# Performance work log

Hardware: AMD Instinct MI355X
Metric: run time of the kernel (lower is better)

## Reference

```python
import jax, jax.numpy as jnp
import numpy as np

LENS = 0.4
DECAY = 0.2
THRESH = 0.2
LOG_SIG_MIN, LOG_SIG_MAX = -20.0, 2.0

# Surrogate-gradient spike: forward is heaviside, backward is rectangular window |x|<lens
@jax.custom_vjp
def act_fun(x):
    return (x > 0.0).astype(x.dtype)

def _act_fwd(x):
    return act_fun(x), x

def _act_bwd(x, g):
    return (g * (jnp.abs(x) < LENS).astype(g.dtype),)

act_fun.defvjp(_act_fwd, _act_bwd)


def _xavier(k, shape):
    fan_out, fan_in = shape
    lim = float(np.sqrt(6.0 / (fan_in + fan_out)))
    return jax.random.uniform(k, shape, jnp.float32, -lim, lim)


def setup_inputs() -> dict:
    key = jax.random.key(0)
    ks = jax.random.split(key, 9)
    B, IN, H, A = 4096, 512, 2048, 32
    return {
        "state": jax.random.normal(ks[0], (B, 5, IN), jnp.float32),
        "W_lif": _xavier(ks[1], (H, IN)), "b_lif": jnp.zeros((H,), jnp.float32),
        "W11": _xavier(ks[2], (H, H)), "b11": jnp.zeros((H,), jnp.float32),
        "W12": _xavier(ks[3], (H, H)), "b12": jnp.zeros((H,), jnp.float32),
        "W21": _xavier(ks[4], (H, H)), "b21": jnp.zeros((H,), jnp.float32),
        "W22": _xavier(ks[5], (H, H)), "b22": jnp.zeros((H,), jnp.float32),
        "Wm": _xavier(ks[6], (A, H)), "bm": jnp.zeros((A,), jnp.float32),
        "Wls": _xavier(ks[7], (A, H)), "bls": jnp.zeros((A,), jnp.float32),
    }


def reference(state, W_lif, b_lif, W11, b11, W12, b12, W21, b21, W22, b22, Wm, bm, Wls, bls):
    x_seq = jnp.repeat(state, 3, axis=1)
    # precompute fc(x) for all steps in one GEMM: [B,15,H]
    fc = jnp.einsum('bti,hi->bth', x_seq, W_lif) + b_lif
    B, T, H = fc.shape

    def step(carry, fc_t):
        mem, spike = carry
        mem1 = mem * DECAY * (1.0 - spike) + fc_t
        spike1 = act_fun(mem1 - THRESH)
        return (mem1, spike1), spike1

    init = (jnp.zeros((B, H), fc.dtype), jnp.zeros((B, H), fc.dtype))
    _, spikes = jax.lax.scan(step, init, jnp.swapaxes(fc, 0, 1))  # [T,B,H]
    x = jnp.mean(spikes, axis=0)  # [B,H]

    x1 = jax.nn.relu(x @ W11.T + b11)
    x1 = jax.nn.relu(x1 @ W12.T + b12)
    mean = x1 @ Wm.T + bm

    x2 = jax.nn.relu(x @ W21.T + b21)
    x2 = jax.nn.relu(x2 @ W22.T + b22)
    log_std = jnp.clip(x2 @ Wls.T + bls, LOG_SIG_MIN, LOG_SIG_MAX)
    return mean, log_std
```

## Files before the change

### kernel.cpp

```cpp
#include <hip/hip_runtime.h>
#include <hip/hip_bf16.h>


typedef _Float16 f16;
using f32x4 = __attribute__((ext_vector_type(4))) float;
using f16x8 = __attribute__((ext_vector_type(8))) f16;

#define MFMA16(a, b, c) __builtin_amdgcn_mfma_f32_16x16x32_f16((a), (b), (c), 0, 0, 0)
#define VMW8()  asm volatile("s_waitcnt vmcnt(8)" ::: "memory")
#define VMW6()  asm volatile("s_waitcnt vmcnt(6)" ::: "memory")
#define VMW0()  asm volatile("s_waitcnt vmcnt(0)" ::: "memory")
#define LGKM0() asm volatile("s_waitcnt lgkmcnt(0)" ::: "memory")
#define BARRIER() __builtin_amdgcn_s_barrier()
#define SCHED0() __builtin_amdgcn_sched_barrier(0)

__device__ __forceinline__ void gload16(const void* g, void* l) {
  __builtin_amdgcn_global_load_lds(
      (const __attribute__((address_space(1))) unsigned int*)g,
      (__attribute__((address_space(3))) unsigned int*)l, 16, 0, 0);
}

__device__ __forceinline__ void cvt8(const float4& a, const float4& b, f16* dst) {
  f16x8 d;
  d[0] = (f16)a.x; d[1] = (f16)a.y; d[2] = (f16)a.z; d[3] = (f16)a.w;
  d[4] = (f16)b.x; d[5] = (f16)b.y; d[6] = (f16)b.z; d[7] = (f16)b.w;
  *(f16x8*)dst = d;
}

__global__ __launch_bounds__(256) void cvt2b_kernel(
    const float* __restrict__ s0, f16* __restrict__ d0, int n8a,
    const float* __restrict__ s1, f16* __restrict__ d1, int n8b)
{
  int i = blockIdx.x * 256 + threadIdx.x;
  const float* src; f16* dst; int k;
  if (i < n8a) { src = s0; dst = d0; k = i; }
  else { k = i - n8a; if (k >= n8b) return; src = s1; dst = d1; }
  const float4* s4 = (const float4*)src;
  float4 a = s4[(size_t)k * 2], b = s4[(size_t)k * 2 + 1];
  cvt8(a, b, dst + (size_t)k * 8);
}

__global__ __launch_bounds__(256) void cvt4_kernel(
    const float* __restrict__ w0, const float* __restrict__ w1,
    const float* __restrict__ w2, const float* __restrict__ w3,
    f16* __restrict__ dst)
{
  int i = blockIdx.x * 256 + threadIdx.x;
  int which = i >> 19, k = i & 524287;
  const float* src = (which == 0) ? w0 : (which == 1) ? w1 : (which == 2) ? w2 : w3;
  const float4* s4 = (const float4*)src;
  float4 a = s4[(size_t)k * 2], b = s4[(size_t)k * 2 + 1];
  cvt8(a, b, dst + (size_t)i * 8);
}

__global__ __launch_bounds__(256) void cvt2_kernel(
    const float* __restrict__ s0, const float* __restrict__ s1,
    f16* __restrict__ d0, f16* __restrict__ d1, int n8each)
{
  int i = blockIdx.x * 256 + threadIdx.x;
  const float* src = (i < n8each) ? s0 : s1;
  f16* dst = (i < n8each) ? d0 : d1;
  int k = (i < n8each) ? i : i - n8each;
  if (k >= n8each) return;
  const float4* s4 = (const float4*)src;
  float4 a = s4[(size_t)k * 2], b = s4[(size_t)k * 2 + 1];
  cvt8(a, b, dst + (size_t)k * 8);
}

__global__ __launch_bounds__(512, 1) void lif256_kernel(
    const f16* __restrict__ S,
    const f16* __restrict__ W,
    const float* __restrict__ bl,
    f16* __restrict__ X)
{
  __shared__ alignas(16) f16 lds[73728];

  const int tid = threadIdx.x, wid = tid >> 6, lane = tid & 63;
  const int wg = ((int)blockIdx.x % 8) * 32 + (int)blockIdx.x / 8;
  const int bn = wg & 15, bm = wg >> 4;
  const int b0 = bm * 256, h0 = bn * 128;
  const int wr0 = (wid >> 1) * 64, wc0 = (wid & 1) * 64;
  const int fr = lane & 15, fq = lane >> 4;
  const int sr = tid >> 3, scb = (tid & 7) * 16;

  f32x4 acc[4][4] = {};
  float mem[4][4][4] = {};
  unsigned pcnt[4][4] = {};

  char* Lb = (char*)&lds[0];
  const int xsw = (fr & 7) << 4;
  const int x0 = (fq * 16) ^ xsw;
  const int x1 = (64 + fq * 16) ^ xsw;
  char* const pA0 = Lb + (wr0 + fr) * 128 + x0;
  char* const pA1 = Lb + (wr0 + fr) * 128 + x1;
  char* const pB0 = Lb + 98304 + (wc0 + fr) * 128 + x0;
  char* const pB1 = Lb + 98304 + (wc0 + fr) * 128 + x1;

  const f16* sBase[4]; const f16* wBase[2];
#pragma unroll
  for (int l = 0; l < 4; ++l) {
    const int row = l * 64 + sr;
    const int c2 = scb ^ ((row & 7) << 4);
    sBase[l] = S + (size_t)(b0 + row) * 2560 + (c2 >> 1);
  }
#pragma unroll
  for (int l = 0; l < 2; ++l) {
    const int row = l * 64 + sr;
    const int c2 = scb ^ ((row & 7) << 4);
    wBase[l] = W + (size_t)(h0 + row) * 512 + (c2 >> 1);
  }

  auto STAGE = [&](int soA, int soB, int g) {
    const int koff = (g >> 3) * 512 + (g & 7) * 64;
    const int kw = (g & 7) * 64;
#pragma unroll
    for (int l = 0; l < 4; ++l)
      gload16(sBase[l] + koff, Lb + soA + l * 8192 + tid * 16);
#pragma unroll
    for (int l = 0; l < 2; ++l)
      gload16(wBase[l] + kw, Lb + 98304 + soB + l * 8192 + tid * 16);
  };

  const float bias[4] = { bl[h0 + wc0 + fr],      bl[h0 + wc0 + 16 + fr],
                          bl[h0 + wc0 + 32 + fr], bl[h0 + wc0 + 48 + fr] };

  STAGE(0, 0, 0);
  STAGE(32768, 16384, 1);
  VMW6();
  BARRIER();
  SCHED0();

  int soA = 0, soB = 0;
  int soStA = 65536, soStB = 32768;
  for (int g = 0; g < 40; ++g) {
    if (g + 2 < 40) STAGE(soStA, soStB, g + 2);
    SCHED0();

    f16x8 b[4][2], a[4][2];
#pragma unroll
    for (int nf = 0; nf < 4; ++nf) {
      b[nf][0] = *(const f16x8*)(pB0 + soB + nf * 2048);
      b[nf][1] = *(const f16x8*)(pB1 + soB + nf * 2048);
    }
#pragma unroll
    for (int mf = 0; mf < 4; ++mf) {
      a[mf][0] = *(const f16x8*)(pA0 + soA + mf * 2048);
      a[mf][1] = *(const f16x8*)(pA1 + soA + mf * 2048);
    }

    __builtin_amdgcn_s_setprio(1);
#pragma unroll
    for (int mf = 0; mf < 4; ++mf)
#pragma unroll
      for (int nf = 0; nf < 4; ++nf) {
        acc[mf][nf] = MFMA16(a[mf][0], b[nf][0], acc[mf][nf]);
        acc[mf][nf] = MFMA16(a[mf][1], b[nf][1], acc[mf][nf]);
      }
    __builtin_amdgcn_s_setprio(0);

    if ((g & 7) == 7) {
#pragma unroll
      for (int mf = 0; mf < 4; ++mf)
#pragma unroll
        for (int nf = 0; nf < 4; ++nf) {
          unsigned pc = pcnt[mf][nf];
#pragma unroll
          for (int r = 0; r < 4; ++r) {
            const float fc = acc[mf][nf][r] + bias[nf];
            float m = mem[mf][nf][r];
            const unsigned inc = 1u << (8 * r);
#pragma unroll
            for (int j = 0; j < 3; ++j) {
              m = ((m > 0.2f) ? 0.f : m * 0.2f) + fc;
              pc += (m > 0.2f) ? inc : 0u;
            }
            mem[mf][nf][r] = m;
          }
          pcnt[mf][nf] = pc;
          acc[mf][nf] = f32x4{0.f, 0.f, 0.f, 0.f};
        }
    }

    LGKM0();
    if (g + 2 < 40)      { VMW6(); }
    else if (g + 1 < 40) { VMW0(); }
    BARRIER();
    SCHED0();

    soA   = (soA   == 65536) ? 0 : soA   + 32768;
    soB   = (soB   == 32768) ? 0 : soB   + 16384;
    soStA = (soStA == 65536) ? 0 : soStA + 32768;
    soStB = (soStB == 32768) ? 0 : soStB + 16384;
  }

#pragma unroll
  for (int nf = 0; nf < 4; ++nf) {
    const int col = h0 + wc0 + nf * 16 + fr;
#pragma unroll
    for (int mf = 0; mf < 4; ++mf) {
      const int row0 = b0 + wr0 + mf * 16 + fq * 4;
#pragma unroll
      for (int r = 0; r < 4; ++r) {
        const float c = (float)((pcnt[mf][nf] >> (8 * r)) & 255u);
        X[(size_t)(row0 + r) * 2048 + col] = (f16)(c / 15.0f);
      }
    }
  }
}

__global__ __launch_bounds__(512, 2) void trunk256_kernel(
    const f16* __restrict__ A0, const f16* __restrict__ A1, int lda,
    const f16* __restrict__ W0, const f16* __restrict__ W1,
    const float* __restrict__ bb0, const float* __restrict__ bb1,
    f16* __restrict__ C0, f16* __restrict__ C1, int ldc,
    int nbm, int nbn_half, int K)
{
  __shared__ alignas(16) f16 lds[4][256 * 64];

  const int tid = threadIdx.x, wid = tid >> 6, lane = tid & 63;
  const int nwg = nbm * nbn_half * 2, q8 = nwg / 8;
  const int wg = ((int)blockIdx.x % 8) * q8 + (int)blockIdx.x / 8;
  const int bmi = wg % nbm, t = wg / nbm;
  const int half = (t >= nbn_half);
  const f16* Ap = half ? A1 : A0;
  const f16* Wp = half ? W1 : W0;
  const float* bias = half ? bb1 : bb0;
  f16* C = half ? C1 : C0;
  const int bm0 = bmi * 256;
  const int bn0 = (half ? t - nbn_half : t) * 256;

  const int wr0 = (wid >> 2) * 128, wc0 = (wid & 3) * 64;
  const int fr = lane & 15, fq = lane >> 4;
  const int sr = tid >> 3, scb = (tid & 7) * 16;

  f32x4 acc[8][4] = {};
  const int NT = K / 64;

  char* Lb = (char*)&lds[0][0];
  const int xsw = (fr & 7) << 4;
  const int x0 = (fq * 16) ^ xsw;
  const int x1 = (64 + fq * 16) ^ xsw;
  char* const pA0 = Lb + (wr0 + fr) * 128 + x0;
  char* const pA1 = Lb + (wr0 + fr) * 128 + x1;
  char* const pB0 = Lb + 65536 + (wc0 + fr) * 128 + x0;
  char* const pB1 = Lb + 65536 + (wc0 + fr) * 128 + x1;

  const f16* aBase[4]; const f16* wBase[4];
#pragma unroll
  for (int l = 0; l < 4; ++l) {
    const int row = l * 64 + sr;
    const int c2 = scb ^ ((row & 7) << 4);
    aBase[l] = Ap + (size_t)(bm0 + row) * lda + (c2 >> 1);
    wBase[l] = Wp + (size_t)(bn0 + row) * K + (c2 >> 1);
  }

  auto STAGE_A = [&](int slot, int kt) {
    const int koff = kt * 64;
#pragma unroll
    for (int l = 0; l < 4; ++l)
      gload16(aBase[l] + koff, Lb + slot * 32768 + l * 8192 + tid * 16);
  };
  auto STAGE_B = [&](int slot, int kt) {
    const int koff = kt * 64;
#pragma unroll
    for (int l = 0; l < 4; ++l)
      gload16(wBase[l] + koff, Lb + 65536 + slot * 32768 + l * 8192 + tid * 16);
  };

  STAGE_A(0, 0); STAGE_B(0, 0);
  STAGE_A(1, 1); STAGE_B(1, 1);
  VMW8();
  BARRIER();
  SCHED0();

#pragma unroll 2
  for (int kt = 0; kt < NT; ++kt) {
    const int slot = kt & 1;
    const int so = slot * 32768;

    auto QUAD = [&](int mbase, f16x8 (&b)[4][2], f16x8 (&a)[2][2]) {
      __builtin_amdgcn_s_setprio(1);
#pragma unroll
      for (int nf = 0; nf < 4; ++nf) {
        acc[mbase][nf]     = MFMA16(a[0][0], b[nf][0], acc[mbase][nf]);
        acc[mbase][nf]     = MFMA16(a[0][1], b[nf][1], acc[mbase][nf]);
        acc[mbase + 1][nf] = MFMA16(a[1][0], b[nf][0], acc[mbase + 1][nf]);
        acc[mbase + 1][nf] = MFMA16(a[1][1], b[nf][1], acc[mbase + 1][nf]);
      }
      __builtin_amdgcn_s_setprio(0);
    };

    f16x8 b[4][2], a0[2][2], a1[2][2];
#pragma unroll
    for (int nf = 0; nf < 4; ++nf) {
      b[nf][0] = *(const f16x8*)(pB0 + so + nf * 2048);
      b[nf][1] = *(const f16x8*)(pB1 + so + nf * 2048);
    }
#pragma unroll
    for (int i = 0; i < 2; ++i) {
      a0[i][0] = *(const f16x8*)(pA0 + so + i * 2048);
      a0[i][1] = *(const f16x8*)(pA1 + so + i * 2048);
    }
    LGKM0();
    BARRIER();
    if (kt + 2 < NT) STAGE_B(slot, kt + 2);
    SCHED0();

#pragma unroll
    for (int i = 0; i < 2; ++i) {
      a1[i][0] = *(const f16x8*)(pA0 + so + (2 + i) * 2048);
      a1[i][1] = *(const f16x8*)(pA1 + so + (2 + i) * 2048);
    }
    QUAD(0, b, a0);
    LGKM0(); SCHED0();
#pragma unroll
    for (int i = 0; i < 2; ++i) {
      a0[i][0] = *(const f16x8*)(pA0 + so + (4 + i) * 2048);
      a0[i][1] = *(const f16x8*)(pA1 + so + (4 + i) * 2048);
    }
    QUAD(2, b, a1);
    LGKM0(); SCHED0();
#pragma unroll
    for (int i = 0; i < 2; ++i) {
      a1[i][0] = *(const f16x8*)(pA0 + so + (6 + i) * 2048);
      a1[i][1] = *(const f16x8*)(pA1 + so + (6 + i) * 2048);
    }
    QUAD(4, b, a0);
    LGKM0();
    BARRIER();
    if (kt + 2 < NT) STAGE_A(slot, kt + 2);
    SCHED0();
    QUAD(6, b, a1);
    if (kt + 2 < NT)      { VMW8(); }
    else if (kt + 1 < NT) { VMW0(); }
    BARRIER();
    SCHED0();
  }

#pragma unroll
  for (int nf = 0; nf < 4; ++nf) {
    const int col = bn0 + wc0 + nf * 16 + fr;
    const float bv = bias[col];
#pragma unroll
    for (int m = 0; m < 8; ++m) {
      const int row0 = bm0 + wr0 + m * 16 + fq * 4;
#pragma unroll
      for (int r = 0; r < 4; ++r) {
        float v = fmaxf(acc[m][nf][r] + bv, 0.f);
        C[(size_t)(row0 + r) * ldc + col] = (f16)v;
      }
    }
  }
}

__global__ __launch_bounds__(256) void head_kernel(
    const f16* __restrict__ H1, const f16* __restrict__ H2,
    const f16* __restrict__ Wm, const float* __restrict__ bm,
    const f16* __restrict__ Wls, const float* __restrict__ bls,
    float* __restrict__ OUT, int M, int K)
{
  const int tid = threadIdx.x, wid = tid >> 6, lane = tid & 63;
  const int m0 = blockIdx.x * 64 + wid * 16;
  const int kb = (lane >> 4) * 8, fr = lane & 15, fq = lane >> 4;

  f32x4 a1[2] = {}, a2[2] = {};
  for (int k0 = 0; k0 < K; k0 += 32) {
    f16x8 f1 = *(const f16x8*)&H1[(size_t)(m0 + fr) * K + k0 + kb];
    f16x8 f2 = *(const f16x8*)&H2[(size_t)(m0 + fr) * K + k0 + kb];
#pragma unroll
    for (int n = 0; n < 2; ++n) {
      f16x8 wm = *(const f16x8*)&Wm[(size_t)(n * 16 + fr) * K + k0 + kb];
      f16x8 wl = *(const f16x8*)&Wls[(size_t)(n * 16 + fr) * K + k0 + kb];
      a1[n] = MFMA16(f1, wm, a1[n]);
      a2[n] = MFMA16(f2, wl, a2[n]);
    }
  }

#pragma unroll
  for (int n = 0; n < 2; ++n) {
    const int col = n * 16 + fr;
    const float bvm = bm[col];
    const float bvl = bls[col];
#pragma unroll
    for (int r = 0; r < 4; ++r) {
      const int row = m0 + fq * 4 + r;
      OUT[(size_t)row * 32 + col] = a1[n][r] + bvm;
      float lv = a2[n][r] + bvl;
      OUT[(size_t)M * 32 + (size_t)row * 32 + col] = fminf(fmaxf(lv, -20.f), 2.f);
    }
  }
}

extern "C" void kernel_launch(void* const* d_in, const int* in_sizes, int n_in,
                              void* d_out, int out_size, void* d_ws, size_t ws_size,
                              hipStream_t stream) {
  const float* state = (const float*)d_in[0];
  const float* W_lif = (const float*)d_in[1];
  const float* b_lif = (const float*)d_in[2];
  const float* W11   = (const float*)d_in[3];
  const float* b11   = (const float*)d_in[4];
  const float* W12   = (const float*)d_in[5];
  const float* b12   = (const float*)d_in[6];
  const float* W21   = (const float*)d_in[7];
  const float* b21   = (const float*)d_in[8];
  const float* W22   = (const float*)d_in[9];
  const float* b22   = (const float*)d_in[10];
  const float* Wm    = (const float*)d_in[11];
  const float* bm    = (const float*)d_in[12];
  const float* Wls   = (const float*)d_in[13];
  const float* bls   = (const float*)d_in[14];
  float* out = (float*)d_out;

  const int B = 4096, IN = 512, H = 2048;
  char* ws = (char*)d_ws;
  f16* x    = (f16*)(ws);
  f16* h1   = (f16*)(ws + 16777216);
  f16* h2   = (f16*)(ws + 33554432);
  f16* s16  = (f16*)(ws + 50331648);
  f16* wl16 = (f16*)(ws + 71303168);
  f16* w4   = (f16*)(ws + 50331648);
  f16* w11h = (f16*)(ws + 50331648);
  f16* w21h = (f16*)(ws + 58720256);
  f16* w12h = (f16*)(ws + 67108864);
  f16* w22h = (f16*)(ws + 75497472);
  f16* h22  = (f16*)(ws + 50331648);
  f16* wmh  = (f16*)(ws + 67108864);
  f16* wlsh = (f16*)(ws + 67239936);
  f16* h12  = x;

  const int n8s = B * 5 * IN / 8, n8w = H * IN / 8;
  cvt2b_kernel<<<(n8s + n8w + 255) / 256, 256, 0, stream>>>(
      state, s16, n8s, W_lif, wl16, n8w);

  lif256_kernel<<<256, 512, 0, stream>>>(s16, wl16, b_lif, x);

  cvt4_kernel<<<4 * 524288 / 256, 256, 0, stream>>>(W11, W21, W12, W22, w4);

  trunk256_kernel<<<256, 512, 0, stream>>>(x, x, H, w11h, w21h, b11, b21,
                                           h1, h2, H, 16, 8, H);
  trunk256_kernel<<<256, 512, 0, stream>>>(h1, h2, H, w12h, w22h, b12, b22,
                                           h12, h22, H, 16, 8, H);

  cvt2_kernel<<<2 * (32 * H / 8) / 256, 256, 0, stream>>>(Wm, Wls, wmh, wlsh, 32 * H / 8);
  head_kernel<<<B / 64, 256, 0, stream>>>(h12, h22, wmh, bm, wlsh, bls, out, B, H);
}
```

Baseline: 259.9 us.

## Prefetch next k-tile LDS fragments during last MFMA quad and merge A/B staging

```diff
diff --git a/kernel.cpp b/kernel.cpp
--- a/kernel.cpp
+++ b/kernel.cpp
@@ -10,6 +10,7 @@
 #define VMW8()  asm volatile("s_waitcnt vmcnt(8)" ::: "memory")
 #define VMW6()  asm volatile("s_waitcnt vmcnt(6)" ::: "memory")
 #define VMW0()  asm volatile("s_waitcnt vmcnt(0)" ::: "memory")
+#define LGKM4() asm volatile("s_waitcnt lgkmcnt(4)" ::: "memory")
 #define LGKM0() asm volatile("s_waitcnt lgkmcnt(0)" ::: "memory")
 #define BARRIER() __builtin_amdgcn_s_barrier()
 #define SCHED0() __builtin_amdgcn_sched_barrier(0)
@@ -254,88 +255,98 @@
     wBase[l] = Wp + (size_t)(bn0 + row) * K + (c2 >> 1);
   }
 
-  auto STAGE_A = [&](int slot, int kt) {
+  auto STAGE_AB = [&](int so, int kt) {
     const int koff = kt * 64;
 #pragma unroll
     for (int l = 0; l < 4; ++l)
-      gload16(aBase[l] + koff, Lb + slot * 32768 + l * 8192 + tid * 16);
+      gload16(aBase[l] + koff, Lb + so + l * 8192 + tid * 16);
+#pragma unroll
+    for (int l = 0; l < 4; ++l)
+      gload16(wBase[l] + koff, Lb + 65536 + so + l * 8192 + tid * 16);
   };
-  auto STAGE_B = [&](int slot, int kt) {
-    const int koff = kt * 64;
-#pragma unroll
-    for (int l = 0; l < 4; ++l)
-      gload16(wBase[l] + koff, Lb + 65536 + slot * 32768 + l * 8192 + tid * 16);
+
+  auto QUAD = [&](int mbase, f16x8 (&bq)[4][2], f16x8 (&a)[2][2]) {
+    __builtin_amdgcn_s_setprio(1);
+#pragma unroll
+    for (int nf = 0; nf < 4; ++nf) {
+      acc[mbase][nf]     = MFMA16(a[0][0], bq[nf][0], acc[mbase][nf]);
+      acc[mbase][nf]     = MFMA16(a[0][1], bq[nf][1], acc[mbase][nf]);
+      acc[mbase + 1][nf] = MFMA16(a[1][0], bq[nf][0], acc[mbase + 1][nf]);
+      acc[mbase + 1][nf] = MFMA16(a[1][1], bq[nf][1], acc[mbase + 1][nf]);
+    }
+    __builtin_amdgcn_s_setprio(0);
   };
 
-  STAGE_A(0, 0); STAGE_B(0, 0);
-  STAGE_A(1, 1); STAGE_B(1, 1);
+  STAGE_AB(0, 0);
+  STAGE_AB(32768, 1);
   VMW8();
   BARRIER();
   SCHED0();
 
-#pragma unroll 2
-  for (int kt = 0; kt < NT; ++kt) {
-    const int slot = kt & 1;
-    const int so = slot * 32768;
-
-    auto QUAD = [&](int mbase, f16x8 (&b)[4][2], f16x8 (&a)[2][2]) {
-      __builtin_amdgcn_s_setprio(1);
-#pragma unroll
-      for (int nf = 0; nf < 4; ++nf) {
-        acc[mbase][nf]     = MFMA16(a[0][0], b[nf][0], acc[mbase][nf]);
-        acc[mbase][nf]     = MFMA16(a[0][1], b[nf][1], acc[mbase][nf]);
-        acc[mbase + 1][nf] = MFMA16(a[1][0], b[nf][0], acc[mbase + 1][nf]);
-        acc[mbase + 1][nf] = MFMA16(a[1][1], b[nf][1], acc[mbase + 1][nf]);
-      }
-      __builtin_amdgcn_s_setprio(0);
-    };
-
-    f16x8 b[4][2], a0[2][2], a1[2][2];
-#pragma unroll
-    for (int nf = 0; nf < 4; ++nf) {
-      b[nf][0] = *(const f16x8*)(pB0 + so + nf * 2048);
-      b[nf][1] = *(const f16x8*)(pB1 + so + nf * 2048);
-    }
-#pragma unroll
-    for (int i = 0; i < 2; ++i) {
-      a0[i][0] = *(const f16x8*)(pA0 + so + i * 2048);
-      a0[i][1] = *(const f16x8*)(pA1 + so + i * 2048);
-    }
-    LGKM0();
-    BARRIER();
-    if (kt + 2 < NT) STAGE_B(slot, kt + 2);
-    SCHED0();
-
-#pragma unroll
-    for (int i = 0; i < 2; ++i) {
-      a1[i][0] = *(const f16x8*)(pA0 + so + (2 + i) * 2048);
-      a1[i][1] = *(const f16x8*)(pA1 + so + (2 + i) * 2048);
-    }
-    QUAD(0, b, a0);
-    LGKM0(); SCHED0();
-#pragma unroll
-    for (int i = 0; i < 2; ++i) {
-      a0[i][0] = *(const f16x8*)(pA0 + so + (4 + i) * 2048);
-      a0[i][1] = *(const f16x8*)(pA1 + so + (4 + i) * 2048);
-    }
-    QUAD(2, b, a1);
-    LGKM0(); SCHED0();
-#pragma unroll
-    for (int i = 0; i < 2; ++i) {
-      a1[i][0] = *(const f16x8*)(pA0 + so + (6 + i) * 2048);
-      a1[i][1] = *(const f16x8*)(pA1 + so + (6 + i) * 2048);
-    }
-    QUAD(4, b, a0);
-    LGKM0();
-    BARRIER();
-    if (kt + 2 < NT) STAGE_A(slot, kt + 2);
-    SCHED0();
-    QUAD(6, b, a1);
-    if (kt + 2 < NT)      { VMW8(); }
-    else if (kt + 1 < NT) { VMW0(); }
-    BARRIER();
-    SCHED0();
-  }
+  f16x8 bbE[4][2], bbO[4][2], aaE[2][2], aaO[2][2];
+#pragma unroll
+  for (int nf = 0; nf < 4; ++nf) {
+    bbE[nf][0] = *(const f16x8*)(pB0 + nf * 2048);
+    bbE[nf][1] = *(const f16x8*)(pB1 + nf * 2048);
+  }
+#pragma unroll
+  for (int i = 0; i < 2; ++i) {
+    aaE[i][0] = *(const f16x8*)(pA0 + i * 2048);
+    aaE[i][1] = *(const f16x8*)(pA1 + i * 2048);
+  }
+
+#define TRUNK_BODY(kt, SO, SON, BC, AC, BF, AF)                               \
+  {                                                                           \
+    f16x8 a1[2][2], a2[2][2];                                                 \
+    _Pragma("unroll")                                                         \
+    for (int i = 0; i < 2; ++i) {                                             \
+      a1[i][0] = *(const f16x8*)(pA0 + SO + (2 + i) * 2048);                  \
+      a1[i][1] = *(const f16x8*)(pA1 + SO + (2 + i) * 2048);                  \
+    }                                                                         \
+    LGKM4(); SCHED0();                                                        \
+    QUAD(0, BC, AC);                                                          \
+    _Pragma("unroll")                                                         \
+    for (int i = 0; i < 2; ++i) {                                             \
+      a2[i][0] = *(const f16x8*)(pA0 + SO + (4 + i) * 2048);                  \
+      a2[i][1] = *(const f16x8*)(pA1 + SO + (4 + i) * 2048);                  \
+    }                                                                         \
+    LGKM4(); SCHED0();                                                        \
+    QUAD(2, BC, a1);                                                          \
+    _Pragma("unroll")                                                         \
+    for (int i = 0; i < 2; ++i) {                                             \
+      a1[i][0] = *(const f16x8*)(pA0 + SO + (6 + i) * 2048);                  \
+      a1[i][1] = *(const f16x8*)(pA1 + SO + (6 + i) * 2048);                  \
+    }                                                                         \
+    LGKM4(); SCHED0();                                                        \
+    QUAD(4, BC, a2);                                                          \
+    LGKM0();                                                                  \
+    BARRIER();                                   \
+    SCHED0();                                                                 \
+    if ((kt) + 2 < NT) { STAGE_AB(SO, (kt) + 2); VMW8(); }                    \
+    else if ((kt) + 1 < NT) { VMW0(); }                                       \
+    BARRIER();                              \
+    SCHED0();                                                                 \
+    if ((kt) + 1 < NT) {                                                      \
+      _Pragma("unroll")                                                       \
+      for (int nf = 0; nf < 4; ++nf) {                                        \
+        BF[nf][0] = *(const f16x8*)(pB0 + SON + nf * 2048);                   \
+        BF[nf][1] = *(const f16x8*)(pB1 + SON + nf * 2048);                   \
+      }                                                                       \
+      _Pragma("unroll")                                                       \
+      for (int i = 0; i < 2; ++i) {                                           \
+        AF[i][0] = *(const f16x8*)(pA0 + SON + i * 2048);                     \
+        AF[i][1] = *(const f16x8*)(pA1 + SON + i * 2048);                     \
+      }                                                                       \
+    }                                                                         \
+    QUAD(6, BC, a1);                    \
+  }
+
+  for (int it = 0; it < NT / 2; ++it) {
+    const int ktE = 2 * it, ktO = 2 * it + 1;
+    TRUNK_BODY(ktE, 0,     32768, bbE, aaE, bbO, aaO);
+    TRUNK_BODY(ktO, 32768, 0,     bbO, aaO, bbE, aaE);
+  }
+#undef TRUNK_BODY
 
 #pragma unroll
   for (int nf = 0; nf < 4; ++nf) {
```

Result: slower. 449.3 us (+72.9%).
